# Optimization experiments

Hardware: AMD Instinct MI355X
Metric: run time of the kernel (lower is better)

The kernel has to match this reference:

```python
import jax, jax.numpy as jnp
import numpy as np

B, H, L, D = 8, 12, 2048, 64
E = H * D            # 768 = state_size = hidden_size
K, S, P = 3, 2, 1    # conv kernel, stride, padding (2P - K = -1 matches avg_pool residual)


def setup_inputs() -> dict:
    key = jax.random.key(0)
    ks = jax.random.split(key, 8)
    init = lambda k, shape: jax.random.normal(k, shape, jnp.float32) * 0.02
    return {
        "state": jax.random.normal(ks[0], (B, H, L, D), jnp.float32),
        # input_proj Linear(E,E)
        "Wi": init(ks[1], (E, E)), "bi": jnp.zeros((E,), jnp.float32),
        # ConvMultiheadAttention: strided Conv1d query proj, stored as [K, E_in, E_out]
        "Wq": init(ks[2], (K, E, E)), "bq": jnp.zeros((E,), jnp.float32),
        "Wk": init(ks[3], (E, E)), "bk": jnp.zeros((E,), jnp.float32),
        "Wv": init(ks[4], (E, E)), "bv": jnp.zeros((E,), jnp.float32),
        "Wao": init(ks[5], (E, E)), "bao": jnp.zeros((E,), jnp.float32),  # attn out_proj
        # output_proj Linear(E,E)
        "Wo": init(ks[6], (E, E)), "bo": jnp.zeros((E,), jnp.float32),
    }


def reference(state, Wi, bi, Wq, bq, Wk, bk, Wv, bv, Wao, bao, Wo, bo):
    b, h, l, d = state.shape
    e = h * d
    # [B,H,L,D] -> [B,L,H*D]
    x = state.transpose(0, 2, 1, 3).reshape(b, l, e)
    residual = x
    # input projection + ReLU
    x = jax.nn.relu(x @ Wi.T + bi)
    # strided convolutional query projection: [B,L,E] -> [B,Lq,E]
    q = jax.lax.conv_general_dilated(
        x, Wq, window_strides=(S,), padding=[(P, P)],
        dimension_numbers=("NWC", "WIO", "NWC")) + bq
    k = x @ Wk.T + bk
    v = x @ Wv.T + bv
    lq = q.shape[1]
    qh = q.reshape(b, lq, h, d)
    kh = k.reshape(b, l, h, d)
    vh = v.reshape(b, l, h, d)
    scale = 1.0 / jnp.sqrt(jnp.asarray(d, x.dtype))
    scores = jnp.einsum("bqhd,bkhd->bhqk", qh, kh) * scale  # [B,H,Lq,L]
    attn = jax.nn.softmax(scores, axis=-1)
    o = jnp.einsum("bhqk,bkhd->bqhd", attn, vh).reshape(b, lq, e)
    o = o @ Wao.T + bao          # attention out_proj
    o = jax.nn.relu(o)
    o = o @ Wo.T + bo            # output projection
    # avg_pool1d with kernel=1, stride=S, pad=0 == strided subsampling
    o = o + residual[:, ::S, :]
    # [B,Lq,E] -> [B,H,Lq,D]
    out = o.reshape(b, lq, h, d).transpose(0, 2, 1, 3)
    return out
```

## Files before the change

kernel.cpp:

```cpp
#include <hip/hip_runtime.h>
#include <hip/hip_bf16.h>
#include <stdint.h>

#define DEVI __device__ __forceinline__

typedef short s8v __attribute__((ext_vector_type(8)));
typedef short s4v __attribute__((ext_vector_type(4)));
typedef float f4v __attribute__((ext_vector_type(4)));

DEVI short f2bf(float f) {
  unsigned u = __builtin_bit_cast(unsigned, f);
  u += 0x7FFFu + ((u >> 16) & 1u);
  return (short)(u >> 16);
}

DEVI void gload16(const void* g, void* l) {
  __builtin_amdgcn_global_load_lds((const __attribute__((address_space(1))) unsigned*)g,
                                   (__attribute__((address_space(3))) unsigned*)l,
                                   16, 0, 0);
}


__global__ __launch_bounds__(256) void k_tr_state(const float* __restrict__ st,
                                                  short* __restrict__ xbf) {
  int idx = blockIdx.x * 256 + threadIdx.x;
  int dc = idx & 7;
  int l  = (idx >> 3) & 2047;
  int hb = idx >> 14;
  int h = hb % 12, b = hb / 12;
  const float* s = st + ((size_t)hb * 2048 + l) * 64 + dc * 8;
  f4v a = *(const f4v*)s;
  f4v c = *(const f4v*)(s + 4);
  short o[8];
#pragma unroll
  for (int j = 0; j < 4; ++j) { o[j] = f2bf(a[j]); o[4 + j] = f2bf(c[j]); }
  *(s8v*)(xbf + ((size_t)(b * 2048 + l)) * 768 + h * 64 + dc * 8) = *(s8v*)o;
}

__global__ __launch_bounds__(256) void k_castw(const float* __restrict__ src,
                                               short* __restrict__ dst) {
  int idx = blockIdx.x * 256 + threadIdx.x;
  const float* s = src + (size_t)idx * 8;
  f4v a = *(const f4v*)s;
  f4v c = *(const f4v*)(s + 4);
  short o[8];
#pragma unroll
  for (int j = 0; j < 4; ++j) { o[j] = f2bf(a[j]); o[4 + j] = f2bf(c[j]); }
  *(s8v*)(dst + (size_t)idx * 8) = *(s8v*)o;
}

__global__ __launch_bounds__(256) void k_tr_wq(const float* __restrict__ wq,
                                               short* __restrict__ wqt) {
  __shared__ float tile[32][33];
  const int kw = blockIdx.z;
  const int i0 = blockIdx.y * 32, o0 = blockIdx.x * 32;
  const int tx = threadIdx.x & 31, ty = threadIdx.x >> 5;
#pragma unroll
  for (int rr = 0; rr < 32; rr += 8)
    tile[ty + rr][tx] = wq[((size_t)kw * 768 + i0 + ty + rr) * 768 + o0 + tx];
  __syncthreads();
#pragma unroll
  for (int rr = 0; rr < 32; rr += 8)
    wqt[(size_t)(o0 + ty + rr) * 2304 + kw * 768 + i0 + tx] = f2bf(tile[tx][ty + rr]);
}

__global__ __launch_bounds__(256) void k_tr_v(const short* __restrict__ v,
                                              short* __restrict__ vt) {
  __shared__ short tile[32][33];
  const int bh = blockIdx.z;
  const int l0 = blockIdx.x * 32, d0 = blockIdx.y * 32;
  const int b = bh / 12, h = bh % 12;
  const int tx = threadIdx.x & 31, ty = threadIdx.x >> 5;
#pragma unroll
  for (int rr = 0; rr < 32; rr += 8)
    tile[ty + rr][tx] = v[((size_t)(b * 2048 + l0 + ty + rr)) * 768 + h * 64 + d0 + tx];
  __syncthreads();
#pragma unroll
  for (int rr = 0; rr < 32; rr += 8)
    vt[((size_t)(bh * 64 + d0 + ty + rr)) * 2048 + l0 + tx] = tile[tx][ty + rr];
}

template <int AMODE, int EPI>
__global__ __launch_bounds__(256, 2)
void k_gemm(const short* __restrict__ A, const short* __restrict__ Bt,
            const float* __restrict__ bias, short* __restrict__ Cbf,
            float* __restrict__ Cf, const float* __restrict__ st,
            const short* __restrict__ zp, int M, int N, int K) {
  __shared__ __align__(16) short As[128 * 32];
  __shared__ __align__(16) short Bs[128 * 32];
  const int tid = threadIdx.x;
  const int w = tid >> 6, l = tid & 63;
  const int g = l >> 4, r = l & 15;

  const int nwg = gridDim.x * gridDim.y;
  const int lin = blockIdx.y * gridDim.x + blockIdx.x;
  const int lin2 = (lin & 7) * (nwg >> 3) + (lin >> 3);
  const int m0 = (lin2 / gridDim.x) * 128, n0 = (lin2 % gridDim.x) * 128;
  const int wm = w >> 1, wn = w & 1;

  f4v acc[4][4] = {};

  const int srow = 16 * w + (l >> 2);
  const int sc8 = 8 * (l & 3);

  const int nsteps = K >> 5;
  for (int ks = 0; ks < nsteps; ++ks) {
    const int kk = ks << 5;
    __syncthreads();
    if (AMODE == 0) {
      const short* a0 = A + ((size_t)(m0 + srow) * K + kk + sc8);
      gload16(a0, (char*)As + w * 1024);
      gload16(a0 + (size_t)64 * K, (char*)As + w * 1024 + 4096);
    } else {
      const int kw = ks / 24;
      const int ii = (ks - kw * 24) * 32 + sc8;
#pragma unroll
      for (int j = 0; j < 2; ++j) {
        int m = m0 + srow + 64 * j;
        int b = m >> 10, t = m & 1023;
        int lpos = 2 * t - 1 + kw;
        const short* a0 = (lpos < 0) ? (zp + sc8)
                                     : A + ((size_t)(b * 2048 + lpos) * 768 + ii);
        gload16(a0, (char*)As + w * 1024 + j * 4096);
      }
    }
    {
      const short* b0 = Bt + ((size_t)(n0 + srow) * K + kk + sc8);
      gload16(b0, (char*)Bs + w * 1024);
      gload16(b0 + (size_t)64 * K, (char*)Bs + w * 1024 + 4096);
    }
    __syncthreads();
    s8v af[4], bfr[4];
#pragma unroll
    for (int mt = 0; mt < 4; ++mt)
      af[mt] = *(const s8v*)&As[(64 * wm + 16 * mt + r) * 32 + 8 * g];
#pragma unroll
    for (int nt = 0; nt < 4; ++nt)
      bfr[nt] = *(const s8v*)&Bs[(64 * wn + 16 * nt + r) * 32 + 8 * g];
#pragma unroll
    for (int mt = 0; mt < 4; ++mt)
#pragma unroll
      for (int nt = 0; nt < 4; ++nt)
        acc[mt][nt] = __builtin_amdgcn_mfma_f32_16x16x32_bf16(af[mt], bfr[nt],
                                                              acc[mt][nt], 0, 0, 0);
  }
#pragma unroll
  for (int nt = 0; nt < 4; ++nt) {
    const int col = n0 + 64 * wn + 16 * nt + r;
    const float bv = bias[col];
#pragma unroll
    for (int mt = 0; mt < 4; ++mt) {
#pragma unroll
      for (int i = 0; i < 4; ++i) {
        int row = m0 + 64 * wm + 16 * mt + 4 * g + i;
        float v = acc[mt][nt][i] + bv;
        if (EPI == 0) v = fmaxf(v, 0.f);
        if (EPI <= 1) {
          Cbf[(size_t)row * N + col] = f2bf(v);
        } else {
          int b = row >> 10, t = row & 1023;
          int h = col >> 6, dd = col & 63;
          float res = st[(((size_t)(b * 12 + h) * 2048) + 2 * t) * 64 + dd];
          Cf[(((size_t)(b * 12 + h) * 1024) + t) * 64 + dd] = v + res;
        }
      }
    }
  }
}

__global__ __launch_bounds__(256, 3)
void k_attn(const short* __restrict__ qb, const short* __restrict__ kb,
            const short* __restrict__ vt, short* __restrict__ ob) {
  __shared__ __align__(16) short Ks[2][64 * 64];
  __shared__ __align__(16) short Vts[2][64 * 64];
  __shared__ __align__(16) short Ps[4][16 * 72];

  const int lin = blockIdx.x;
  const int blk = (lin & 7) * 192 + (lin >> 3);
  const int qblk = blk & 15, bh = blk >> 4;
  const int b = bh / 12, h = bh % 12;
  const int tid = threadIdx.x;
  const int w = tid >> 6, l = tid & 63;
  const int g = l >> 4, r = l & 15;
  const int row = tid >> 3, p = tid & 7;

  const short* qrow = qb + ((size_t)(b * 1024 + qblk * 64 + 16 * w + r)) * 768 + h * 64;
  s8v qf[2];
  qf[0] = *(const s8v*)(qrow + 8 * g);
  qf[1] = *(const s8v*)(qrow + 32 + 8 * g);

  auto STAGE = [&](int buf, int jb) {
#pragma unroll
    for (int iss = 0; iss < 2; ++iss) {
      int jr = row + 32 * iss;
      int c = p ^ (jr & 7);
      gload16(kb + ((size_t)(b * 2048 + jb * 64 + jr)) * 768 + h * 64 + 8 * c,
              (char*)Ks[buf] + iss * 4096 + w * 1024);
      gload16(vt + ((size_t)(bh * 64 + jr)) * 2048 + jb * 64 + 8 * c,
              (char*)Vts[buf] + iss * 4096 + w * 1024);
    }
  };

  f4v oacc[4] = {};
  float mrun = -3.0e38f, lrun = 0.f;

  STAGE(0, 0);
  asm volatile("s_waitcnt vmcnt(0)" ::: "memory");
  __builtin_amdgcn_s_barrier();

  for (int jb = 0; jb < 32; ++jb) {
    const int cur = jb & 1;
    if (jb < 31) STAGE(cur ^ 1, jb + 1);

    f4v sacc[4] = {};
#pragma unroll
    for (int nt = 0; nt < 4; ++nt)
#pragma unroll
      for (int c = 0; c < 2; ++c) {
        s8v kf = *(const s8v*)&Ks[cur][(16 * nt + r) * 64 + 8 * ((4 * c + g) ^ (r & 7))];
        sacc[nt] = __builtin_amdgcn_mfma_f32_16x16x32_bf16(kf, qf[c], sacc[nt], 0, 0, 0);
      }

    float s[16];
    float mx = -3.0e38f;
#pragma unroll
    for (int nt = 0; nt < 4; ++nt)
#pragma unroll
      for (int i = 0; i < 4; ++i) {
        s[4 * nt + i] = sacc[nt][i] * 0.125f;
        mx = fmaxf(mx, s[4 * nt + i]);
      }
    mx = fmaxf(mx, __shfl_xor(mx, 16));
    mx = fmaxf(mx, __shfl_xor(mx, 32));

    bool defer = __all(mx <= mrun + 8.0f);
    float mn = defer ? mrun : fmaxf(mrun, mx);
    float alpha = defer ? 1.0f : __expf(mrun - mn);
    mrun = mn;

    float ls = 0.f;
#pragma unroll
    for (int k = 0; k < 8; ++k) {
      float p0 = __expf(s[2 * k] - mn);
      float p1 = __expf(s[2 * k + 1] - mn);
      ls += p0 + p1;
      unsigned pw = ((unsigned)(unsigned short)f2bf(p1) << 16) |
                    (unsigned)(unsigned short)f2bf(p0);
      *(unsigned*)&Ps[w][r * 72 + 16 * (k >> 1) + 4 * g + 2 * (k & 1)] = pw;
    }
    ls += __shfl_xor(ls, 16);
    ls += __shfl_xor(ls, 32);
    lrun = lrun * alpha + ls;
    if (!defer) {
#pragma unroll
      for (int mt = 0; mt < 4; ++mt)
#pragma unroll
        for (int i = 0; i < 4; ++i) oacc[mt][i] *= alpha;
    }

    asm volatile("" ::: "memory");
    s8v pf[2];
#pragma unroll
    for (int kc = 0; kc < 2; ++kc)
      pf[kc] = *(const s8v*)&Ps[w][r * 72 + 32 * kc + 8 * g];
#pragma unroll
    for (int mt = 0; mt < 4; ++mt)
#pragma unroll
      for (int kc = 0; kc < 2; ++kc) {
        s8v vf = *(const s8v*)&Vts[cur][(16 * mt + r) * 64 + 8 * ((4 * kc + g) ^ (r & 7))];
        oacc[mt] = __builtin_amdgcn_mfma_f32_16x16x32_bf16(vf, pf[kc], oacc[mt], 0, 0, 0);
      }

    asm volatile("s_waitcnt vmcnt(0)" ::: "memory");
    __builtin_amdgcn_s_barrier();
  }

  const float inv = 1.f / lrun;
  short* obase = ob + ((size_t)(b * 1024 + qblk * 64 + 16 * w + r)) * 768 + h * 64;
#pragma unroll
  for (int mt = 0; mt < 4; ++mt) {
    short o4[4];
#pragma unroll
    for (int i = 0; i < 4; ++i) o4[i] = f2bf(oacc[mt][i] * inv);
    *(s4v*)(obase + 16 * mt + 4 * g) = *(s4v*)o4;
  }
}

extern "C" void kernel_launch(void* const* d_in, const int* in_sizes, int n_in,
                              void* d_out, int out_size, void* d_ws, size_t ws_size,
                              hipStream_t stream) {
  const float* state = (const float*)d_in[0];
  const float* Wi  = (const float*)d_in[1];
  const float* bi  = (const float*)d_in[2];
  const float* Wq  = (const float*)d_in[3];
  const float* bq  = (const float*)d_in[4];
  const float* Wk  = (const float*)d_in[5];
  const float* bk  = (const float*)d_in[6];
  const float* Wv  = (const float*)d_in[7];
  const float* bv  = (const float*)d_in[8];
  const float* Wao = (const float*)d_in[9];
  const float* bao = (const float*)d_in[10];
  const float* Wo  = (const float*)d_in[11];
  const float* bo  = (const float*)d_in[12];
  float* out = (float*)d_out;

  char* ws = (char*)d_ws;
  const size_t SZ = (size_t)16384 * 768 * 2;
  short* xbf = (short*)ws;
  short* y   = (short*)(ws + SZ);
  short* kbf = (short*)(ws + 2 * SZ);
  short* vbf = (short*)(ws + 3 * SZ);
  short* qbf = (short*)(ws + 4 * SZ);
  char*  wp  = ws + 4 * SZ + SZ / 2;
  short* wib  = (short*)wp;
  short* wkb  = (short*)(wp + 1 * 1179648);
  short* wvb  = (short*)(wp + 2 * 1179648);
  short* waob = (short*)(wp + 3 * 1179648);
  short* wob  = (short*)(wp + 4 * 1179648);
  short* wqt  = (short*)(wp + 5 * 1179648);
  short* zp   = (short*)(wp + 5 * 1179648 + 3538944);
  short* vtb   = xbf;
  short* attno = y;
  short* z1    = (short*)((char*)y + SZ / 2);

  hipMemsetAsync(zp, 0, 256, stream);
  k_tr_state<<<6144, 256, 0, stream>>>(state, xbf);
  k_castw<<<288, 256, 0, stream>>>(Wi, wib);
  k_castw<<<288, 256, 0, stream>>>(Wk, wkb);
  k_castw<<<288, 256, 0, stream>>>(Wv, wvb);
  k_castw<<<288, 256, 0, stream>>>(Wao, waob);
  k_castw<<<288, 256, 0, stream>>>(Wo, wob);
  k_tr_wq<<<dim3(24, 24, 3), 256, 0, stream>>>(Wq, wqt);

  k_gemm<0, 0><<<dim3(6, 128), 256, 0, stream>>>(xbf, wib, bi, y, nullptr, nullptr, zp, 16384, 768, 768);
  k_gemm<0, 1><<<dim3(6, 128), 256, 0, stream>>>(y, wkb, bk, kbf, nullptr, nullptr, zp, 16384, 768, 768);
  k_gemm<0, 1><<<dim3(6, 128), 256, 0, stream>>>(y, wvb, bv, vbf, nullptr, nullptr, zp, 16384, 768, 768);
  k_gemm<1, 1><<<dim3(6, 64), 256, 0, stream>>>(y, wqt, bq, qbf, nullptr, nullptr, zp, 8192, 768, 2304);
  k_tr_v<<<dim3(64, 2, 96), 256, 0, stream>>>(vbf, vtb);
  k_attn<<<1536, 256, 0, stream>>>(qbf, kbf, vtb, attno);
  k_gemm<0, 0><<<dim3(6, 64), 256, 0, stream>>>(attno, waob, bao, z1, nullptr, nullptr, zp, 8192, 768, 768);
  k_gemm<0, 2><<<dim3(6, 64), 256, 0, stream>>>(z1, wob, bo, nullptr, out, state, zp, 8192, 768, 768);
}
```

Measured before the change: 438.9 us.

## Fuse K/V projections, fold softmax scale into Wk, tune attention kernel

K and V projections are merged into one GEMM with N=1536 over concatenated weights (wkb and wvb are contiguous) and a combined bias. The 1/sqrt(d) scale is folded into Wk and bk, which removes the per-score multiply. The attention kernel also gets a hardware packed bf16 convert, a swizzled unpadded P buffer in LDS, precomputed LDS pointers, a tree max reduction, and a launch bound of 4 waves. The intent is to cut launch count, redundant reads of y, and ALU and LDS overhead in attention; the cost is more register pressure and small bf16 rounding differences from the pre-scaled weights.

```diff
diff --git a/kernel.cpp b/kernel.cpp
--- a/kernel.cpp
+++ b/kernel.cpp
@@ -12,6 +12,12 @@
   unsigned u = __builtin_bit_cast(unsigned, f);
   u += 0x7FFFu + ((u >> 16) & 1u);
   return (short)(u >> 16);
+}
+
+DEVI unsigned cvtpk(float lo, float hi) {
+  unsigned r;
+  asm("v_cvt_pk_bf16_f32 %0, %1, %2" : "=v"(r) : "v"(lo), "v"(hi));
+  return r;
 }
 
 DEVI void gload16(const void* g, void* l) {
@@ -38,15 +44,22 @@
 }
 
 __global__ __launch_bounds__(256) void k_castw(const float* __restrict__ src,
-                                               short* __restrict__ dst) {
+                                               short* __restrict__ dst, float sc) {
   int idx = blockIdx.x * 256 + threadIdx.x;
   const float* s = src + (size_t)idx * 8;
   f4v a = *(const f4v*)s;
   f4v c = *(const f4v*)(s + 4);
   short o[8];
 #pragma unroll
-  for (int j = 0; j < 4; ++j) { o[j] = f2bf(a[j]); o[4 + j] = f2bf(c[j]); }
+  for (int j = 0; j < 4; ++j) { o[j] = f2bf(a[j] * sc); o[4 + j] = f2bf(c[j] * sc); }
   *(s8v*)(dst + (size_t)idx * 8) = *(s8v*)o;
+}
+
+__global__ __launch_bounds__(256) void k_bkv(const float* __restrict__ bk,
+                                             const float* __restrict__ bv,
+                                             float* __restrict__ bkv) {
+  int i = blockIdx.x * 256 + threadIdx.x;
+  bkv[i] = (i < 768) ? bk[i] * 0.125f : bv[i - 768];
 }
 
 __global__ __launch_bounds__(256) void k_tr_wq(const float* __restrict__ wq,
@@ -65,7 +78,7 @@
 }
 
 __global__ __launch_bounds__(256) void k_tr_v(const short* __restrict__ v,
-                                              short* __restrict__ vt) {
+                                              short* __restrict__ vt, int vs) {
   __shared__ short tile[32][33];
   const int bh = blockIdx.z;
   const int l0 = blockIdx.x * 32, d0 = blockIdx.y * 32;
@@ -73,7 +86,7 @@
   const int tx = threadIdx.x & 31, ty = threadIdx.x >> 5;
 #pragma unroll
   for (int rr = 0; rr < 32; rr += 8)
-    tile[ty + rr][tx] = v[((size_t)(b * 2048 + l0 + ty + rr)) * 768 + h * 64 + d0 + tx];
+    tile[ty + rr][tx] = v[((size_t)(b * 2048 + l0 + ty + rr)) * vs + h * 64 + d0 + tx];
   __syncthreads();
 #pragma unroll
   for (int rr = 0; rr < 32; rr += 8)
@@ -168,12 +181,12 @@
   }
 }
 
-__global__ __launch_bounds__(256, 3)
-void k_attn(const short* __restrict__ qb, const short* __restrict__ kb,
+__global__ __launch_bounds__(256, 4)
+void k_attn(const short* __restrict__ qb, const short* __restrict__ kvb,
             const short* __restrict__ vt, short* __restrict__ ob) {
   __shared__ __align__(16) short Ks[2][64 * 64];
   __shared__ __align__(16) short Vts[2][64 * 64];
-  __shared__ __align__(16) short Ps[4][16 * 72];
+  __shared__ __align__(16) short Ps[4][16 * 64];
 
   const int lin = blockIdx.x;
   const int blk = (lin & 7) * 192 + (lin >> 3);
@@ -189,12 +202,24 @@
   qf[0] = *(const s8v*)(qrow + 8 * g);
   qf[1] = *(const s8v*)(qrow + 32 + 8 * g);
 
+  unsigned* pswr[8];
+#pragma unroll
+  for (int k = 0; k < 8; ++k) {
+    const int nt = k >> 1, t = k & 1;
+    pswr[k] = (unsigned*)&Ps[w][r * 64 + 8 * ((2 * nt + (g >> 1) + r) & 7) +
+                               4 * (g & 1) + 2 * t];
+  }
+  const s8v* psrd[2];
+#pragma unroll
+  for (int kc = 0; kc < 2; ++kc)
+    psrd[kc] = (const s8v*)&Ps[w][r * 64 + 8 * ((4 * kc + g + r) & 7)];
+
   auto STAGE = [&](int buf, int jb) {
 #pragma unroll
     for (int iss = 0; iss < 2; ++iss) {
       int jr = row + 32 * iss;
       int c = p ^ (jr & 7);
-      gload16(kb + ((size_t)(b * 2048 + jb * 64 + jr)) * 768 + h * 64 + 8 * c,
+      gload16(kvb + ((size_t)(b * 2048 + jb * 64 + jr)) * 1536 + h * 64 + 8 * c,
               (char*)Ks[buf] + iss * 4096 + w * 1024);
       gload16(vt + ((size_t)(bh * 64 + jr)) * 2048 + jb * 64 + 8 * c,
               (char*)Vts[buf] + iss * 4096 + w * 1024);
@@ -222,14 +247,15 @@
       }
 
     float s[16];
-    float mx = -3.0e38f;
 #pragma unroll
     for (int nt = 0; nt < 4; ++nt)
 #pragma unroll
-      for (int i = 0; i < 4; ++i) {
-        s[4 * nt + i] = sacc[nt][i] * 0.125f;
-        mx = fmaxf(mx, s[4 * nt + i]);
-      }
+      for (int i = 0; i < 4; ++i) s[4 * nt + i] = sacc[nt][i];
+    float m01 = fmaxf(fmaxf(s[0], s[1]), fmaxf(s[2], s[3]));
+    float m23 = fmaxf(fmaxf(s[4], s[5]), fmaxf(s[6], s[7]));
+    float m45 = fmaxf(fmaxf(s[8], s[9]), fmaxf(s[10], s[11]));
+    float m67 = fmaxf(fmaxf(s[12], s[13]), fmaxf(s[14], s[15]));
+    float mx = fmaxf(fmaxf(m01, m23), fmaxf(m45, m67));
     mx = fmaxf(mx, __shfl_xor(mx, 16));
     mx = fmaxf(mx, __shfl_xor(mx, 32));
 
@@ -244,9 +270,7 @@
       float p0 = __expf(s[2 * k] - mn);
       float p1 = __expf(s[2 * k + 1] - mn);
       ls += p0 + p1;
-      unsigned pw = ((unsigned)(unsigned short)f2bf(p1) << 16) |
-                    (unsigned)(unsigned short)f2bf(p0);
-      *(unsigned*)&Ps[w][r * 72 + 16 * (k >> 1) + 4 * g + 2 * (k & 1)] = pw;
+      *pswr[k] = cvtpk(p0, p1);
     }
     ls += __shfl_xor(ls, 16);
     ls += __shfl_xor(ls, 32);
@@ -259,17 +283,14 @@
     }
 
     asm volatile("" ::: "memory");
-    s8v pf[2];
-#pragma unroll
-    for (int kc = 0; kc < 2; ++kc)
-      pf[kc] = *(const s8v*)&Ps[w][r * 72 + 32 * kc + 8 * g];
-#pragma unroll
-    for (int mt = 0; mt < 4; ++mt)
-#pragma unroll
-      for (int kc = 0; kc < 2; ++kc) {
-        s8v vf = *(const s8v*)&Vts[cur][(16 * mt + r) * 64 + 8 * ((4 * kc + g) ^ (r & 7))];
-        oacc[mt] = __builtin_amdgcn_mfma_f32_16x16x32_bf16(vf, pf[kc], oacc[mt], 0, 0, 0);
-      }
+    s8v pf0 = *psrd[0], pf1 = *psrd[1];
+#pragma unroll
+    for (int mt = 0; mt < 4; ++mt) {
+      s8v vf0 = *(const s8v*)&Vts[cur][(16 * mt + r) * 64 + 8 * ((g) ^ (r & 7))];
+      s8v vf1 = *(const s8v*)&Vts[cur][(16 * mt + r) * 64 + 8 * ((4 + g) ^ (r & 7))];
+      oacc[mt] = __builtin_amdgcn_mfma_f32_16x16x32_bf16(vf0, pf0, oacc[mt], 0, 0, 0);
+      oacc[mt] = __builtin_amdgcn_mfma_f32_16x16x32_bf16(vf1, pf1, oacc[mt], 0, 0, 0);
+    }
 
     asm volatile("s_waitcnt vmcnt(0)" ::: "memory");
     __builtin_amdgcn_s_barrier();
@@ -279,10 +300,10 @@
   short* obase = ob + ((size_t)(b * 1024 + qblk * 64 + 16 * w + r)) * 768 + h * 64;
 #pragma unroll
   for (int mt = 0; mt < 4; ++mt) {
-    short o4[4];
-#pragma unroll
-    for (int i = 0; i < 4; ++i) o4[i] = f2bf(oacc[mt][i] * inv);
-    *(s4v*)(obase + 16 * mt + 4 * g) = *(s4v*)o4;
+    uint2 uu;
+    uu.x = cvtpk(oacc[mt][0] * inv, oacc[mt][1] * inv);
+    uu.y = cvtpk(oacc[mt][2] * inv, oacc[mt][3] * inv);
+    *(uint2*)(obase + 16 * mt + 4 * g) = uu;
   }
 }
 
@@ -308,8 +329,7 @@
   const size_t SZ = (size_t)16384 * 768 * 2;
   short* xbf = (short*)ws;
   short* y   = (short*)(ws + SZ);
-  short* kbf = (short*)(ws + 2 * SZ);
-  short* vbf = (short*)(ws + 3 * SZ);
+  short* kvbf = (short*)(ws + 2 * SZ);
   short* qbf = (short*)(ws + 4 * SZ);
   char*  wp  = ws + 4 * SZ + SZ / 2;
   short* wib  = (short*)wp;
@@ -319,25 +339,26 @@
   short* wob  = (short*)(wp + 4 * 1179648);
   short* wqt  = (short*)(wp + 5 * 1179648);
   short* zp   = (short*)(wp + 5 * 1179648 + 3538944);
+  float* bkv  = (float*)(wp + 5 * 1179648 + 3538944 + 512);
   short* vtb   = xbf;
   short* attno = y;
   short* z1    = (short*)((char*)y + SZ / 2);
 
   hipMemsetAsync(zp, 0, 256, stream);
   k_tr_state<<<6144, 256, 0, stream>>>(state, xbf);
-  k_castw<<<288, 256, 0, stream>>>(Wi, wib);
-  k_castw<<<288, 256, 0, stream>>>(Wk, wkb);
-  k_castw<<<288, 256, 0, stream>>>(Wv, wvb);
-  k_castw<<<288, 256, 0, stream>>>(Wao, waob);
-  k_castw<<<288, 256, 0, stream>>>(Wo, wob);
+  k_castw<<<288, 256, 0, stream>>>(Wi, wib, 1.0f);
+  k_castw<<<288, 256, 0, stream>>>(Wk, wkb, 0.125f);
+  k_castw<<<288, 256, 0, stream>>>(Wv, wvb, 1.0f);
+  k_castw<<<288, 256, 0, stream>>>(Wao, waob, 1.0f);
+  k_castw<<<288, 256, 0, stream>>>(Wo, wob, 1.0f);
+  k_bkv<<<6, 256, 0, stream>>>(bk, bv, bkv);
   k_tr_wq<<<dim3(24, 24, 3), 256, 0, stream>>>(Wq, wqt);
 
   k_gemm<0, 0><<<dim3(6, 128), 256, 0, stream>>>(xbf, wib, bi, y, nullptr, nullptr, zp, 16384, 768, 768);
-  k_gemm<0, 1><<<dim3(6, 128), 256, 0, stream>>>(y, wkb, bk, kbf, nullptr, nullptr, zp, 16384, 768, 768);
-  k_gemm<0, 1><<<dim3(6, 128), 256, 0, stream>>>(y, wvb, bv, vbf, nullptr, nullptr, zp, 16384, 768, 768);
+  k_gemm<0, 1><<<dim3(12, 128), 256, 0, stream>>>(y, wkb, bkv, kvbf, nullptr, nullptr, zp, 16384, 1536, 768);
   k_gemm<1, 1><<<dim3(6, 64), 256, 0, stream>>>(y, wqt, bq, qbf, nullptr, nullptr, zp, 8192, 768, 2304);
-  k_tr_v<<<dim3(64, 2, 96), 256, 0, stream>>>(vbf, vtb);
-  k_attn<<<1536, 256, 0, stream>>>(qbf, kbf, vtb, attno);
+  k_tr_v<<<dim3(64, 2, 96), 256, 0, stream>>>(kvbf + 768, vtb, 1536);
+  k_attn<<<1536, 256, 0, stream>>>(qbf, kvbf, vtb, attno);
   k_gemm<0, 0><<<dim3(6, 64), 256, 0, stream>>>(attno, waob, bao, z1, nullptr, nullptr, zp, 8192, 768, 768);
   k_gemm<0, 2><<<dim3(6, 64), 256, 0, stream>>>(z1, wob, bo, nullptr, out, state, zp, 8192, 768, 768);
 }
```

Result: faster. 423.9 us (-3.4%).
